# Optimization experiments

Measured on AMD Instinct MI355X. Metric: run time of the kernel, lower is better.

## Reference

```python
import jax, jax.numpy as jnp
import numpy as np
from jax import lax

# Module hyper-parameters (match init_kwargs)
NUM_IN = 8       # num_input_capsules
IN_DIM = 16      # input_capsule_dimension
K = 5            # kernel_size (padding=2 => 'same' spatial size)
PAD = 2
NUM_OUT = 8      # num_output_capsules
OUT_DIM = 16     # output_capsules_dimension
ROUTING = 3


def squash(p):
    # p: [..., D]; squash along last dim (matches torch squash with 1e-9 eps)
    p_norm_sq = jnp.sum(p * p, axis=-1, keepdims=True)
    p_norm = jnp.sqrt(p_norm_sq + 1e-9)
    return p_norm_sq / (1.0 + p_norm_sq) * p / p_norm


def setup_inputs() -> dict:
    key = jax.random.key(0)
    k1, k2 = jax.random.split(key)
    N, H, W_sp = 8, 64, 64
    u = jax.random.normal(k1, (N, NUM_IN, IN_DIM, H, W_sp), dtype=jnp.float32)
    # per-input-capsule conv weights, scaled ~1/sqrt(fan_in) for numerical sanity
    W = jax.random.normal(k2, (NUM_IN, NUM_OUT * OUT_DIM, IN_DIM, K, K), dtype=jnp.float32) * 0.05
    return {"u": u, "W": W}


def _forward(u, W):
    N = u.shape[0]

    def conv_one(x, w):  # x: [N,Cin,H,W], w: [OD,Cin,K,K]
        return lax.conv_general_dilated(x, w, window_strides=(1, 1),
                                        padding=[(PAD, PAD), (PAD, PAD)],
                                        dimension_numbers=('NCHW', 'OIHW', 'NCHW'))

    # vmap over the input-capsule axis (each capsule has its own conv)
    u_hat = jax.vmap(conv_one, in_axes=(1, 0))(u, W)          # [I, N, O*D, H, W]
    H, W_sp = u_hat.shape[-2], u_hat.shape[-1]
    u_hat = u_hat.reshape(NUM_IN, N, NUM_OUT, OUT_DIM, H, W_sp)
    u_hat = u_hat.transpose(0, 1, 4, 5, 2, 3)                 # [I, N, H, W, O, D]

    spatial_pad = [(0, 0), (0, 0), (0, 0), (PAD, PAD), (PAD, PAD)]
    b = jnp.zeros((NUM_IN, N, NUM_OUT, H, W_sp), dtype=u_hat.dtype)

    v = None
    for d in range(ROUTING):
        uh = u_hat if d == ROUTING - 1 else lax.stop_gradient(u_hat)
        # local spatial max (KxK, stride 1, -inf pad) then max over output capsules
        b_sp_max = lax.reduce_window(b, -jnp.inf, lax.max,
                                     (1, 1, 1, K, K), (1, 1, 1, 1, 1), spatial_pad)
        b_max = jnp.max(b_sp_max, axis=2, keepdims=True)      # [I, N, 1, H, W]
        c = jnp.exp(b - b_max)                                # [I, N, O, H, W]
        # conv2d_same with all-ones [1,O,K,K] kernel == sum over O and KxK window
        sum_c = lax.reduce_window(c, 0.0, lax.add,
                                  (1, 1, NUM_OUT, K, K), (1, 1, 1, 1, 1), spatial_pad)
        r = c / sum_c                                         # [I, N, O, H, W]
        r_nhwo = r.transpose(0, 1, 3, 4, 2)                   # [I, N, H, W, O]
        p = jnp.einsum('inhwo,inhwod->nhwod', r_nhwo, uh)     # sum over input capsules
        v = squash(p)                                         # [N, H, W, O, D]
        if d < ROUTING - 1:
            agree = jnp.einsum('inhwod,nhwod->inhwo', uh, v)  # [I, N, H, W, O]
            b = b + agree.transpose(0, 1, 4, 2, 3)            # back to [I, N, O, H, W]
    # final transpose_(1,3).transpose_(2,4): [N,H,W,O,D] -> [N,O,D,H,W]
    return v.transpose(0, 3, 4, 1, 2)


def reference(u, W):
    return _forward(u, W)
```

## Files before the change

kernel.cpp:

```cpp
#include <hip/hip_runtime.h>
#include <hip/hip_fp16.h>
#include <cmath>

#define HWS 4096
#define HWP 2048

typedef _Float16 f16x8 __attribute__((ext_vector_type(8)));
typedef float f32x16 __attribute__((ext_vector_type(16)));
typedef unsigned short ushort_t;
typedef ushort_t ushort8 __attribute__((ext_vector_type(8)));
typedef unsigned int uint_t;

static constexpr size_t UHP_OFF = 0;
static constexpr size_t B_OFF   = 16777216ull;
static constexpr size_t WGT_OFF = 18874368ull;
static constexpr size_t WPK_OFF = 20971520ull;

__device__ __forceinline__ float h2f(uint_t u) { return __half2float(__ushort_as_half((ushort_t)u)); }

__global__ __launch_bounds__(256) void wpack_kernel(const float* __restrict__ W,
                                                    ushort_t* __restrict__ wp) {
  const int gid = blockIdx.x * 256 + threadIdx.x;
  const int lane = gid & 63;
  int r = gid >> 6;
  const int oct = r & 3; r >>= 2;
  const int tap = r % 25, i = r / 25;
  const int oc = oct * 32 + (lane & 31);
  const int cin0 = (lane >> 5) * 8;
  ushort8 out;
#pragma unroll
  for (int e = 0; e < 8; ++e) {
    float f = W[(((size_t)i * 128 + oc) * 16 + cin0 + e) * 25 + tap];
    out[e] = __half_as_ushort(__float2half(f));
  }
  *(ushort8*)(wp + (size_t)gid * 8) = out;
}

__global__ __launch_bounds__(512, 4) void conv_kernel(const float* __restrict__ u,
                                                      const ushort_t* __restrict__ wp,
                                                      uint_t* __restrict__ uhp) {
  __shared__ ushort_t ut[8 * 68 * 24];

  const int tid = threadIdx.x;
  const int lane = tid & 63, wid = tid >> 6;
  const int l31 = lane & 31, half = lane >> 5;
  const int wv = wid >> 1, oh = wid & 1;
  const int h0 = blockIdx.x * 4;
  const int q = blockIdx.y;
  const int i = q & 7, n = q >> 3;

  const ushort_t* wbase = wp + (size_t)i * 51200 + (oh * 2) * 512 + lane * 8;

  const float* ub = u + (size_t)q * 16 * HWS;
  {
    const int lane_x = tid & 63;
    const int grp = tid >> 6;
    const int gh = h0 - 2 + grp;
    const bool rowok = (unsigned)gh < 64u;
    const float* src = ub + gh * 64 + lane_x;
    float vals[16];
#pragma unroll
    for (int it = 0; it < 16; ++it)
      vals[it] = rowok ? src[(size_t)it * HWS] : 0.f;
    const int xbase = (grp * 68 + lane_x + 2) * 24;
#pragma unroll
    for (int itp = 0; itp < 8; ++itp) {
      uint_t pk = (uint_t)__half_as_ushort(__float2half(vals[2 * itp])) |
                  ((uint_t)__half_as_ushort(__float2half(vals[2 * itp + 1])) << 16);
      *(uint_t*)&ut[xbase + 2 * itp] = pk;
    }
    if (tid < 256) {
      const int y = tid >> 5, r = tid & 31;
      const int xs = r >> 3, cp = r & 7;
      const int x = (xs < 2) ? xs : (64 + xs);
      *(uint_t*)&ut[(y * 68 + x) * 24 + 2 * cp] = 0u;
    }
  }
  __syncthreads();

  f32x16 acc[2][2];
#pragma unroll
  for (int pt = 0; pt < 2; ++pt)
#pragma unroll
    for (int ot = 0; ot < 2; ++ot)
#pragma unroll
      for (int e = 0; e < 16; ++e) acc[pt][ot][e] = 0.f;

  uint4 wbuf[3][2];
#pragma unroll
  for (int t = 0; t < 2; ++t)
#pragma unroll
    for (int f = 0; f < 2; ++f)
      wbuf[t][f] = *(const uint4*)(wbase + t * 2048 + f * 512);

#pragma unroll
  for (int tap = 0; tap < 25; ++tap) {
    const int kh = tap / 5, kw = tap - kh * 5;
    if (tap + 2 < 25) {
#pragma unroll
      for (int f = 0; f < 2; ++f)
        wbuf[(tap + 2) % 3][f] = *(const uint4*)(wbase + (tap + 2) * 2048 + f * 512);
    }
    f16x8 ah[2];
#pragma unroll
    for (int pt = 0; pt < 2; ++pt)
      ah[pt] = *(const f16x8*)&ut[((wv + kh) * 68 + pt * 32 + l31 + kw) * 24 + half * 8];
#pragma unroll
    for (int ot = 0; ot < 2; ++ot) {
      f16x8 bb = *(const f16x8*)&wbuf[tap % 3][ot];
#pragma unroll
      for (int pt = 0; pt < 2; ++pt)
        acc[pt][ot] = __builtin_amdgcn_mfma_f32_32x32x16_f16(ah[pt], bb, acc[pt][ot], 0, 0, 0);
    }
  }

  const int h = h0 + wv;
  uint_t* uhb = uhp + ((size_t)(n * HWP + h * 32) * 8 + i) * 128;
#pragma unroll
  for (int pt = 0; pt < 2; ++pt)
#pragma unroll
    for (int ot = 0; ot < 2; ++ot) {
      const int otg = oh * 2 + ot;
#pragma unroll
      for (int rp = 0; rp < 8; ++rp) {
        const int r = rp * 2;
        const int xp = pt * 16 + 4 * (rp >> 1) + 2 * half + (rp & 1);
        uint_t lo = (uint_t)__half_as_ushort(__float2half(acc[pt][ot][r]));
        uint_t hi = (uint_t)__half_as_ushort(__float2half(acc[pt][ot][r + 1]));
        uhb[(size_t)xp * 1024 + otg * 32 + l31] = lo | (hi << 16);
      }
    }
}

__global__ __launch_bounds__(256) void fsm_kernel(const float* __restrict__ b,
                                                  float* __restrict__ wgt) {
  __shared__ float bt[8][36][36];
  __shared__ float m1[40][40];
  __shared__ float bm[36][36];
  __shared__ float st[36][36];
  const int tid = threadIdx.x;
  const int i = blockIdx.z >> 3, n = blockIdx.z & 7;
  const int h0 = blockIdx.y * 32, w0 = blockIdx.x * 32;
  const int inb = i * 8 + n;
  const float* bb = b + (size_t)inb * HWS * 8;

  for (int idx = tid; idx < 1600; idx += 256) {
    const int yy = idx / 40, xx = idx - yy * 40;
    const int h = h0 + yy - 4, w = w0 + xx - 4;
    float v[8];
    if ((unsigned)h < 64u && (unsigned)w < 64u) {
      const float4 a = *(const float4*)(bb + (size_t)(h * 64 + w) * 8);
      const float4 c = *(const float4*)(bb + (size_t)(h * 64 + w) * 8 + 4);
      v[0] = a.x; v[1] = a.y; v[2] = a.z; v[3] = a.w;
      v[4] = c.x; v[5] = c.y; v[6] = c.z; v[7] = c.w;
    } else {
#pragma unroll
      for (int o = 0; o < 8; ++o) v[o] = -INFINITY;
    }
    float m = v[0];
#pragma unroll
    for (int o = 1; o < 8; ++o) m = fmaxf(m, v[o]);
    m1[yy][xx] = m;
    if ((unsigned)(yy - 2) < 36u && (unsigned)(xx - 2) < 36u) {
#pragma unroll
      for (int o = 0; o < 8; ++o) bt[o][yy - 2][xx - 2] = v[o];
    }
  }
  __syncthreads();
  for (int idx = tid; idx < 1296; idx += 256) {
    const int ys = idx / 36, xs = idx - ys * 36;
    float m = -INFINITY;
#pragma unroll
    for (int dy = 0; dy < 5; ++dy)
#pragma unroll
      for (int dx = 0; dx < 5; ++dx) m = fmaxf(m, m1[ys + dy][xs + dx]);
    bm[ys][xs] = m;
  }
  __syncthreads();
  for (int idx = tid; idx < 1296; idx += 256) {
    const int ys = idx / 36, xs = idx - ys * 36;
    const float bmv = bm[ys][xs];
    float ss = 0.f;
#pragma unroll
    for (int o = 0; o < 8; ++o) ss += __expf(bt[o][ys][xs] - bmv);
    st[ys][xs] = ss;
  }
  __syncthreads();
  const int tx = tid & 31, ty = tid >> 5;
  for (int p = 0; p < 4; ++p) {
    const int y = ty + p * 8, x = tx;
    float sum = 0.f;
#pragma unroll
    for (int dy = 0; dy < 5; ++dy)
#pragma unroll
      for (int dx = 0; dx < 5; ++dx) sum += st[y + dy][x + dx];
    const float rs = 1.0f / sum;
    const float bmv = bm[y + 2][x + 2];
    float w8[8];
#pragma unroll
    for (int o = 0; o < 8; ++o) w8[o] = __expf(bt[o][y + 2][x + 2] - bmv) * rs;
    float* dst = wgt + (size_t)inb * HWS * 8 + (size_t)((h0 + y) * 64 + (w0 + x)) * 8;
    *(float4*)dst = make_float4(w8[0], w8[1], w8[2], w8[3]);
    *(float4*)(dst + 4) = make_float4(w8[4], w8[5], w8[6], w8[7]);
  }
}

template <int INIT, int FINAL>
__global__ __launch_bounds__(256) void route_kernel(const uint_t* __restrict__ uhp,
                                                    const float* __restrict__ wgt,
                                                    float* __restrict__ b,
                                                    float* __restrict__ out) {
  __shared__ float sm_w[1024];
  __shared__ float sm_b[2048];
  const int tid = threadIdx.x;
  const int quad = tid & 31, slot = tid >> 5;
  const int o = quad >> 2;
  const int n = blockIdx.y;
  const int hw0 = blockIdx.x * 16;
  const int hwp = blockIdx.x * 8 + slot;

  if (!INIT) {
    const int li = tid >> 5, r = tid & 31;
    const int pxl = r >> 1, o4 = (r & 1) * 4;
    const float4 wv4 = *(const float4*)(wgt + ((size_t)(li * 8 + n) * HWS + hw0 + pxl) * 8 + o4);
    *(float4*)&sm_w[(li * 16 + pxl) * 8 + o4] = wv4;
    __syncthreads();
  }

  float uv0[8][4], uv1[8][4];
  float pa0[4] = {0.f, 0.f, 0.f, 0.f}, pa1[4] = {0.f, 0.f, 0.f, 0.f};
  const uint_t* up = uhp + (size_t)(n * HWP + hwp) * 1024 + quad * 4;
#pragma unroll
  for (int i = 0; i < 8; ++i) {
    const uint4 q4 = *(const uint4*)(up + i * 128);
    const uint_t qq[4] = {q4.x, q4.y, q4.z, q4.w};
    float w0 = 1.f, w1 = 1.f;
    if (!INIT) {
      w0 = sm_w[(i * 16 + slot * 2) * 8 + o];
      w1 = sm_w[(i * 16 + slot * 2 + 1) * 8 + o];
    }
#pragma unroll
    for (int e = 0; e < 4; ++e) {
      const float a0 = h2f(qq[e] & 0xffffu);
      const float a1 = h2f(qq[e] >> 16);
      uv0[i][e] = a0;
      uv1[i][e] = a1;
      pa0[e] = fmaf(w0, a0, pa0[e]);
      pa1[e] = fmaf(w1, a1, pa1[e]);
    }
  }
  if (INIT) {
    const int hwa = hw0 + slot * 2;
    const int h = hwa >> 6, x = hwa & 63;
    const int nh = min(h + 2, 63) - max(h - 2, 0) + 1;
    const int nw0 = min(x + 2, 63) - max(x - 2, 0) + 1;
    const int nw1 = min(x + 3, 63) - max(x - 1, 0) + 1;
    const float r0 = 1.0f / (float)(8 * nh * nw0);
    const float r1 = 1.0f / (float)(8 * nh * nw1);
#pragma unroll
    for (int e = 0; e < 4; ++e) { pa0[e] *= r0; pa1[e] *= r1; }
  }
  float ns0 = pa0[0] * pa0[0] + pa0[1] * pa0[1] + pa0[2] * pa0[2] + pa0[3] * pa0[3];
  float ns1 = pa1[0] * pa1[0] + pa1[1] * pa1[1] + pa1[2] * pa1[2] + pa1[3] * pa1[3];
  ns0 += __shfl_xor(ns0, 1); ns0 += __shfl_xor(ns0, 2);
  ns1 += __shfl_xor(ns1, 1); ns1 += __shfl_xor(ns1, 2);
  const float f0 = ns0 / ((1.f + ns0) * sqrtf(ns0 + 1e-9f));
  const float f1 = ns1 / ((1.f + ns1) * sqrtf(ns1 + 1e-9f));
  float v0[4], v1[4];
#pragma unroll
  for (int e = 0; e < 4; ++e) { v0[e] = f0 * pa0[e]; v1[e] = f1 * pa1[e]; }

  if (FINAL) {
#pragma unroll
    for (int e = 0; e < 4; ++e) {
      sm_b[(quad * 4 + e) * 16 + slot * 2] = v0[e];
      sm_b[(quad * 4 + e) * 16 + slot * 2 + 1] = v1[e];
    }
    __syncthreads();
    const int od = tid >> 1, p8 = (tid & 1) * 8;
    float* dst = out + ((size_t)n * 128 + od) * HWS + hw0 + p8;
    const float* src = &sm_b[od * 16 + p8];
    *(float4*)dst = make_float4(src[0], src[1], src[2], src[3]);
    *(float4*)(dst + 4) = make_float4(src[4], src[5], src[6], src[7]);
  } else {
#pragma unroll
    for (int i = 0; i < 8; ++i) {
      float a0 = uv0[i][0] * v0[0] + uv0[i][1] * v0[1] + uv0[i][2] * v0[2] + uv0[i][3] * v0[3];
      float a1 = uv1[i][0] * v1[0] + uv1[i][1] * v1[1] + uv1[i][2] * v1[2] + uv1[i][3] * v1[3];
      a0 += __shfl_xor(a0, 1); a0 += __shfl_xor(a0, 2);
      a1 += __shfl_xor(a1, 1); a1 += __shfl_xor(a1, 2);
      if ((quad & 3) == 0) {
        sm_b[(i * 16 + slot * 2) * 8 + o] = a0;
        sm_b[(i * 16 + slot * 2 + 1) * 8 + o] = a1;
      }
    }
    __syncthreads();
    const int li = tid >> 5, r = tid & 31;
    const int pxl = r >> 1, o4 = (r & 1) * 4;
    float* bp = b + ((size_t)(li * 8 + n) * HWS + hw0 + pxl) * 8 + o4;
    const float4 ag = *(const float4*)&sm_b[(li * 16 + pxl) * 8 + o4];
    if (INIT) {
      *(float4*)bp = ag;
    } else {
      float4 old = *(const float4*)bp;
      *(float4*)bp = make_float4(old.x + ag.x, old.y + ag.y, old.z + ag.z, old.w + ag.w);
    }
  }
}

extern "C" void kernel_launch(void* const* d_in, const int* in_sizes, int n_in,
                              void* d_out, int out_size, void* d_ws, size_t ws_size,
                              hipStream_t stream) {
  const float* u = (const float*)d_in[0];
  const float* W = (const float*)d_in[1];
  float* ws = (float*)d_ws;
  uint_t* uhp = (uint_t*)(ws + UHP_OFF);
  float* b = ws + B_OFF;
  float* wgt = ws + WGT_OFF;
  ushort_t* wpk = (ushort_t*)(ws + WPK_OFF);
  float* out = (float*)d_out;

  wpack_kernel<<<dim3(200), 256, 0, stream>>>(W, wpk);
  conv_kernel<<<dim3(16, 64), 512, 0, stream>>>(u, wpk, uhp);
  route_kernel<1, 0><<<dim3(256, 8), 256, 0, stream>>>(uhp, wgt, b, out);
  fsm_kernel<<<dim3(2, 2, 64), 256, 0, stream>>>(b, wgt);
  route_kernel<0, 0><<<dim3(256, 8), 256, 0, stream>>>(uhp, wgt, b, out);
  fsm_kernel<<<dim3(2, 2, 64), 256, 0, stream>>>(b, wgt);
  route_kernel<0, 1><<<dim3(256, 8), 256, 0, stream>>>(uhp, wgt, b, out);
}
```

Baseline: 110.9 us.

## Process two row tiles per conv block with prefetched second tile and LDS double buffer

Each conv block now handles two 4-row tiles (h0 and h0+32), halving the grid. The second tile's input is loaded from global memory into registers before computing the first tile, then written into a second LDS buffer, so the load latency overlaps with MFMA work. The LDS activation reads are also software-pipelined one tap ahead. In exchange it uses double the LDS and more registers, which may reduce occupancy, and it halves the number of blocks.

```diff
diff --git a/kernel.cpp b/kernel.cpp
--- a/kernel.cpp
+++ b/kernel.cpp
@@ -39,97 +39,132 @@
 __global__ __launch_bounds__(512, 4) void conv_kernel(const float* __restrict__ u,
                                                       const ushort_t* __restrict__ wp,
                                                       uint_t* __restrict__ uhp) {
-  __shared__ ushort_t ut[8 * 68 * 24];
+  __shared__ ushort_t ut[2][8 * 68 * 24];
 
   const int tid = threadIdx.x;
   const int lane = tid & 63, wid = tid >> 6;
   const int l31 = lane & 31, half = lane >> 5;
   const int wv = wid >> 1, oh = wid & 1;
-  const int h0 = blockIdx.x * 4;
+  const int h0A = blockIdx.x * 4;
+  const int h0B = h0A + 32;
   const int q = blockIdx.y;
   const int i = q & 7, n = q >> 3;
 
-  const ushort_t* wbase = wp + (size_t)i * 51200 + (oh * 2) * 512 + lane * 8;
-
+  const ushort_t* wbase = wp + (size_t)i * 51200 + oh * 1024 + lane * 8;
   const float* ub = u + (size_t)q * 16 * HWS;
+  const int lane_x = tid & 63;
+  const int grp = tid >> 6;
+  const int xbase = (grp * 68 + lane_x + 2) * 24;
+
   {
-    const int lane_x = tid & 63;
-    const int grp = tid >> 6;
-    const int gh = h0 - 2 + grp;
+    const int gh = h0A - 2 + grp;
     const bool rowok = (unsigned)gh < 64u;
     const float* src = ub + gh * 64 + lane_x;
     float vals[16];
 #pragma unroll
     for (int it = 0; it < 16; ++it)
       vals[it] = rowok ? src[(size_t)it * HWS] : 0.f;
-    const int xbase = (grp * 68 + lane_x + 2) * 24;
 #pragma unroll
     for (int itp = 0; itp < 8; ++itp) {
       uint_t pk = (uint_t)__half_as_ushort(__float2half(vals[2 * itp])) |
                   ((uint_t)__half_as_ushort(__float2half(vals[2 * itp + 1])) << 16);
-      *(uint_t*)&ut[xbase + 2 * itp] = pk;
-    }
-    if (tid < 256) {
-      const int y = tid >> 5, r = tid & 31;
-      const int xs = r >> 3, cp = r & 7;
-      const int x = (xs < 2) ? xs : (64 + xs);
-      *(uint_t*)&ut[(y * 68 + x) * 24 + 2 * cp] = 0u;
-    }
-  }
-  __syncthreads();
-
-  f32x16 acc[2][2];
-#pragma unroll
-  for (int pt = 0; pt < 2; ++pt)
-#pragma unroll
-    for (int ot = 0; ot < 2; ++ot)
-#pragma unroll
-      for (int e = 0; e < 16; ++e) acc[pt][ot][e] = 0.f;
-
-  uint4 wbuf[3][2];
-#pragma unroll
-  for (int t = 0; t < 2; ++t)
-#pragma unroll
-    for (int f = 0; f < 2; ++f)
-      wbuf[t][f] = *(const uint4*)(wbase + t * 2048 + f * 512);
-
-#pragma unroll
-  for (int tap = 0; tap < 25; ++tap) {
-    const int kh = tap / 5, kw = tap - kh * 5;
-    if (tap + 2 < 25) {
+      *(uint_t*)&ut[0][xbase + 2 * itp] = pk;
+    }
+  }
+  if (tid < 256) {
+    const int y = tid >> 5, r = tid & 31;
+    const int xs = r >> 3, cp = r & 7;
+    const int x = (xs < 2) ? xs : (64 + xs);
+    *(uint_t*)&ut[0][(y * 68 + x) * 24 + 2 * cp] = 0u;
+    *(uint_t*)&ut[1][(y * 68 + x) * 24 + 2 * cp] = 0u;
+  }
+
+  float vB[16];
+  {
+    const int gh = h0B - 2 + grp;
+    const bool rowok = (unsigned)gh < 64u;
+    const float* src = ub + gh * 64 + lane_x;
+#pragma unroll
+    for (int it = 0; it < 16; ++it)
+      vB[it] = rowok ? src[(size_t)it * HWS] : 0.f;
+  }
+  __syncthreads();
+
+  auto compute_tile = [&](const ushort_t* utb, int h0) {
+    f32x16 acc[2][2];
+#pragma unroll
+    for (int pt = 0; pt < 2; ++pt)
+#pragma unroll
+      for (int ot = 0; ot < 2; ++ot)
+#pragma unroll
+        for (int e = 0; e < 16; ++e) acc[pt][ot][e] = 0.f;
+
+    uint4 wbuf[3][2];
+#pragma unroll
+    for (int t = 0; t < 2; ++t)
 #pragma unroll
       for (int f = 0; f < 2; ++f)
-        wbuf[(tap + 2) % 3][f] = *(const uint4*)(wbase + (tap + 2) * 2048 + f * 512);
-    }
-    f16x8 ah[2];
+        wbuf[t][f] = *(const uint4*)(wbase + t * 2048 + f * 512);
+
+    f16x8 ahc[2], ahn[2];
 #pragma unroll
     for (int pt = 0; pt < 2; ++pt)
-      ah[pt] = *(const f16x8*)&ut[((wv + kh) * 68 + pt * 32 + l31 + kw) * 24 + half * 8];
-#pragma unroll
-    for (int ot = 0; ot < 2; ++ot) {
-      f16x8 bb = *(const f16x8*)&wbuf[tap % 3][ot];
-#pragma unroll
-      for (int pt = 0; pt < 2; ++pt)
-        acc[pt][ot] = __builtin_amdgcn_mfma_f32_32x32x16_f16(ah[pt], bb, acc[pt][ot], 0, 0, 0);
-    }
-  }
-
-  const int h = h0 + wv;
-  uint_t* uhb = uhp + ((size_t)(n * HWP + h * 32) * 8 + i) * 128;
-#pragma unroll
-  for (int pt = 0; pt < 2; ++pt)
-#pragma unroll
-    for (int ot = 0; ot < 2; ++ot) {
-      const int otg = oh * 2 + ot;
-#pragma unroll
-      for (int rp = 0; rp < 8; ++rp) {
-        const int r = rp * 2;
-        const int xp = pt * 16 + 4 * (rp >> 1) + 2 * half + (rp & 1);
-        uint_t lo = (uint_t)__half_as_ushort(__float2half(acc[pt][ot][r]));
-        uint_t hi = (uint_t)__half_as_ushort(__float2half(acc[pt][ot][r + 1]));
-        uhb[(size_t)xp * 1024 + otg * 32 + l31] = lo | (hi << 16);
-      }
-    }
+      ahc[pt] = *(const f16x8*)&utb[((wv + 0) * 68 + pt * 32 + l31 + 0) * 24 + half * 8];
+
+#pragma unroll
+    for (int tap = 0; tap < 25; ++tap) {
+      if (tap + 2 < 25) {
+#pragma unroll
+        for (int f = 0; f < 2; ++f)
+          wbuf[(tap + 2) % 3][f] = *(const uint4*)(wbase + (tap + 2) * 2048 + f * 512);
+      }
+      if (tap < 24) {
+        const int tn = tap + 1;
+        const int khn = tn / 5, kwn = tn - khn * 5;
+#pragma unroll
+        for (int pt = 0; pt < 2; ++pt)
+          ahn[pt] = *(const f16x8*)&utb[((wv + khn) * 68 + pt * 32 + l31 + kwn) * 24 + half * 8];
+      }
+#pragma unroll
+      for (int ot = 0; ot < 2; ++ot) {
+        f16x8 bb = *(const f16x8*)&wbuf[tap % 3][ot];
+#pragma unroll
+        for (int pt = 0; pt < 2; ++pt)
+          acc[pt][ot] = __builtin_amdgcn_mfma_f32_32x32x16_f16(ahc[pt], bb, acc[pt][ot], 0, 0, 0);
+      }
+#pragma unroll
+      for (int pt = 0; pt < 2; ++pt) ahc[pt] = ahn[pt];
+    }
+
+    const int h = h0 + wv;
+    uint_t* uhb = uhp + ((size_t)(n * HWP + h * 32) * 8 + i) * 128;
+#pragma unroll
+    for (int pt = 0; pt < 2; ++pt)
+#pragma unroll
+      for (int ot = 0; ot < 2; ++ot) {
+        const int otg = oh * 2 + ot;
+#pragma unroll
+        for (int rp = 0; rp < 8; ++rp) {
+          const int r = rp * 2;
+          const int xp = pt * 16 + 4 * (rp >> 1) + 2 * half + (rp & 1);
+          uint_t lo = (uint_t)__half_as_ushort(__float2half(acc[pt][ot][r]));
+          uint_t hi = (uint_t)__half_as_ushort(__float2half(acc[pt][ot][r + 1]));
+          uhb[(size_t)xp * 1024 + otg * 32 + l31] = lo | (hi << 16);
+        }
+      }
+  };
+
+  compute_tile(ut[0], h0A);
+
+#pragma unroll
+  for (int itp = 0; itp < 8; ++itp) {
+    uint_t pk = (uint_t)__half_as_ushort(__float2half(vB[2 * itp])) |
+                ((uint_t)__half_as_ushort(__float2half(vB[2 * itp + 1])) << 16);
+    *(uint_t*)&ut[1][xbase + 2 * itp] = pk;
+  }
+  __syncthreads();
+
+  compute_tile(ut[1], h0B);
 }
 
 __global__ __launch_bounds__(256) void fsm_kernel(const float* __restrict__ b,
@@ -321,7 +356,7 @@
   float* out = (float*)d_out;
 
   wpack_kernel<<<dim3(200), 256, 0, stream>>>(W, wpk);
-  conv_kernel<<<dim3(16, 64), 512, 0, stream>>>(u, wpk, uhp);
+  conv_kernel<<<dim3(8, 64), 512, 0, stream>>>(u, wpk, uhp);
   route_kernel<1, 0><<<dim3(256, 8), 256, 0, stream>>>(uhp, wgt, b, out);
   fsm_kernel<<<dim3(2, 2, 64), 256, 0, stream>>>(b, wgt);
   route_kernel<0, 0><<<dim3(256, 8), 256, 0, stream>>>(uhp, wgt, b, out);
```

After: 130.2 us. 1.17x slower.
